# Performance work log

Hardware: AMD Instinct MI355X
Metric: run time of the kernel (lower is better)

## Reference

```python
import jax, jax.numpy as jnp
import numpy as np

MAX_LORAS, OUT, IN = 8, 4096, 4096
B, S = 4, 2048


def setup_inputs() -> dict:
    key = jax.random.key(0)
    k1, k2, k3 = jax.random.split(key, 3)
    x = jax.random.normal(k1, (B, S, IN), dtype=jnp.float32)
    weight = jax.random.normal(k2, (MAX_LORAS, OUT, IN), dtype=jnp.float32) * 0.02
    adapter_ids = jax.random.randint(k3, (B,), 0, MAX_LORAS, dtype=jnp.int32)
    return {"x": x, "weight": weight, "adapter_ids": adapter_ids}


def reference(x, weight, adapter_ids):
    # Gather a full [OUT, IN] matrix per batch element (matches weight[adapter_ids]).
    w = weight[adapter_ids]                 # [B, OUT, IN]
    # F.linear(x, w) == x @ w^T, batched over B: [B, S, IN] x [B, OUT, IN] -> [B, S, OUT]
    return jnp.einsum('bsi,boi->bso', x, w)
```

## Files before the change

### kernel.cpp

```cpp
#include <hip/hip_runtime.h>
#include <hip/hip_bf16.h>


#define SEQ    2048
#define IN_K   4096
#define OUT_N  4096
#define NB     4

typedef __attribute__((ext_vector_type(8))) short  short8;
typedef __attribute__((ext_vector_type(4))) float  float4v;

constexpr int BM = 256, BN = 256, BK = 32;
constexpr int GT = 512;
constexpr int KTILES = IN_K / BK;

__device__ inline short f2b(float f) {
    union { float f; unsigned u; } v; v.f = f;
    unsigned r = v.u + 0x7FFFu + ((v.u >> 16) & 1u);
    return (short)(r >> 16);
}
__device__ inline short8 pack8(float4v lo, float4v hi) {
    short8 r;
    r[0] = f2b(lo[0]); r[1] = f2b(lo[1]); r[2] = f2b(lo[2]); r[3] = f2b(lo[3]);
    r[4] = f2b(hi[0]); r[5] = f2b(hi[1]); r[6] = f2b(hi[2]); r[7] = f2b(hi[3]);
    return r;
}

typedef const __attribute__((address_space(1))) void* gp1_t;
typedef __attribute__((address_space(3))) void*       lp3_t;
__device__ inline void gload_lds16(const void* g, void* l) {
    __builtin_amdgcn_global_load_lds((gp1_t)g, (lp3_t)l, 16, 0, 0);
}

#define WAITV(N)  asm volatile("s_waitcnt vmcnt(" #N ")" ::: "memory")
#define WAITL0()  asm volatile("s_waitcnt lgkmcnt(0)" ::: "memory")

__global__ __launch_bounds__(256)
void cvt_x_kernel(const float* __restrict__ x, short* __restrict__ o, int n8)
{
    int i = blockIdx.x * blockDim.x + threadIdx.x;
    const int stride = gridDim.x * blockDim.x;
    for (; i < n8; i += stride) {
        const float4v a = *(const float4v*)(x + (size_t)i * 8);
        const float4v b = *(const float4v*)(x + (size_t)i * 8 + 4);
        *(short8*)(o + (size_t)i * 8) = pack8(a, b);
    }
}

__global__ __launch_bounds__(256)
void cvt_w_kernel(const float* __restrict__ w, const int* __restrict__ ids,
                  short* __restrict__ o, int by_id)
{
    const int b  = blockIdx.y;
    const int id = ids[b];
    int slot = b;
    if (by_id) {
        for (int j = 0; j < b; ++j) if (ids[j] == id) return;
        slot = id;
    }
    const float* __restrict__ src = w + (size_t)id   * OUT_N * IN_K;
    short* __restrict__       dst = o + (size_t)slot * OUT_N * IN_K;
    const int n8 = OUT_N * IN_K / 8;
    int i = blockIdx.x * blockDim.x + threadIdx.x;
    const int stride = gridDim.x * blockDim.x;
    for (; i < n8; i += stride) {
        const float4v a = *(const float4v*)(src + (size_t)i * 8);
        const float4v c = *(const float4v*)(src + (size_t)i * 8 + 4);
        *(short8*)(dst + (size_t)i * 8) = pack8(a, c);
    }
}

__global__ __launch_bounds__(GT, 2)
void mll_gemm_v5(const short* __restrict__ A, const short* __restrict__ W,
                 const int* __restrict__ ids, int by_id, float* __restrict__ out)
{
    __shared__ __align__(16) short lds[4][2 * BM * BK];

    const int tid  = threadIdx.x;
    const int lane = tid & 63;
    const int wid  = tid >> 6;
    const int wr   = wid >> 2;
    const int wc   = wid & 3;

    const int bid = blockIdx.x;
    const int n   = (bid & 7) * 64 + (bid >> 3);
    const int bx  = n & 15;
    const int by  = (n >> 4) & 7;
    const int bz  = n >> 7;
    const int brow = by * BM, bcol = bx * BN;

    const int wslot = by_id ? ids[bz] : bz;
    const short* __restrict__ Ab = A + (size_t)bz * SEQ * IN_K + (size_t)brow * IN_K;
    const short* __restrict__ Bb = W + (size_t)wslot * OUT_N * IN_K + (size_t)bcol * IN_K;

    const int c0 = tid, c1 = tid + GT;
    const int r0_ = c0 >> 2, s0_ = (c0 & 3) ^ ((r0_ >> 1) & 3);
    const int r1_ = c1 >> 2, s1_ = (c1 & 3) ^ ((r1_ >> 1) & 3);
    const short* pa0 = Ab + (size_t)r0_ * IN_K + s0_ * 8;
    const short* pa1 = Ab + (size_t)r1_ * IN_K + s1_ * 8;
    const short* pb0 = Bb + (size_t)r0_ * IN_K + s0_ * 8;
    const short* pb1 = Bb + (size_t)r1_ * IN_K + s1_ * 8;

    float4v acc[8][4];
#pragma unroll
    for (int m = 0; m < 8; ++m)
#pragma unroll
        for (int q = 0; q < 4; ++q)
            acc[m][q] = (float4v){0.f, 0.f, 0.f, 0.f};

    const int lr  = lane & 15;
    const int ksl = lane >> 4;
    const int ks2 = (ksl ^ ((lr >> 1) & 3)) * 8;

#pragma unroll
    for (int tt = 0; tt < 3; ++tt) {
        short* s = &lds[tt][0];
        gload_lds16(pa0 + tt * BK, s + c0 * 8);
        gload_lds16(pa1 + tt * BK, s + c1 * 8);
        gload_lds16(pb0 + tt * BK, s + BM * BK + c0 * 8);
        gload_lds16(pb1 + tt * BK, s + BM * BK + c1 * 8);
    }
    WAITV(8);
    __builtin_amdgcn_s_barrier();

    short8 af_a[4], af_b[4], bf[4];
    {
        const short* sA = &lds[0][0];
        const short* sB = sA + BM * BK;
#pragma unroll
        for (int m = 0; m < 4; ++m)
            af_a[m] = *(const short8*)(sA + (wr * 128 + m * 16 + lr) * BK + ks2);
#pragma unroll
        for (int q = 0; q < 4; ++q)
            bf[q] = *(const short8*)(sB + (wc * 64 + q * 16 + lr) * BK + ks2);
    }

    for (int t = 0; t < KTILES; ++t) {
        const short* sA = &lds[t & 3][0];

        WAITL0();
        __builtin_amdgcn_s_setprio(1);
#pragma unroll
        for (int m = 0; m < 4; ++m)
#pragma unroll
            for (int q = 0; q < 4; ++q)
                acc[m][q] = __builtin_amdgcn_mfma_f32_16x16x32_bf16(
                    af_a[m], bf[q], acc[m][q], 0, 0, 0);
        __builtin_amdgcn_s_setprio(0);
#pragma unroll
        for (int m = 0; m < 4; ++m)
            af_b[m] = *(const short8*)(sA + (wr * 128 + (m + 4) * 16 + lr) * BK + ks2);
        if (t <= KTILES - 4) {
            short* d = &lds[(t + 3) & 3][0];
            gload_lds16(pa0 + (t + 3) * BK, d + c0 * 8);
            gload_lds16(pa1 + (t + 3) * BK, d + c1 * 8);
        }
        if (t <= KTILES - 4)      WAITV(6);
        else if (t == KTILES - 3) WAITV(4);
        else if (t == KTILES - 2) WAITV(0);
        __builtin_amdgcn_s_barrier();

        WAITL0();
        __builtin_amdgcn_s_setprio(1);
#pragma unroll
        for (int m = 0; m < 4; ++m)
#pragma unroll
            for (int q = 0; q < 4; ++q)
                acc[m + 4][q] = __builtin_amdgcn_mfma_f32_16x16x32_bf16(
                    af_b[m], bf[q], acc[m + 4][q], 0, 0, 0);
        __builtin_amdgcn_s_setprio(0);
        if (t < KTILES - 1) {
            const short* sN = &lds[(t + 1) & 3][0];
            const short* sNB = sN + BM * BK;
#pragma unroll
            for (int m = 0; m < 4; ++m)
                af_a[m] = *(const short8*)(sN + (wr * 128 + m * 16 + lr) * BK + ks2);
#pragma unroll
            for (int q = 0; q < 4; ++q)
                bf[q] = *(const short8*)(sNB + (wc * 64 + q * 16 + lr) * BK + ks2);
        }
        if (t <= KTILES - 4) {
            short* d = &lds[(t + 3) & 3][0];
            gload_lds16(pb0 + (t + 3) * BK, d + BM * BK + c0 * 8);
            gload_lds16(pb1 + (t + 3) * BK, d + BM * BK + c1 * 8);
        }
        __builtin_amdgcn_s_barrier();
    }

    float* __restrict__ ob = out + (size_t)bz * SEQ * OUT_N;
    const int lrow = ksl * 4;
#pragma unroll
    for (int m = 0; m < 8; ++m) {
#pragma unroll
        for (int q = 0; q < 4; ++q) {
            const int r0 = brow + wr * 128 + m * 16 + lrow;
            const int c  = bcol + wc * 64 + q * 16 + lr;
#pragma unroll
            for (int j = 0; j < 4; ++j)
                ob[(size_t)(r0 + j) * OUT_N + c] = acc[m][q][j];
        }
    }
}

__device__ inline int xr(int row) { return (row & 3) ^ ((row >> 2) & 3); }

__global__ __launch_bounds__(256, 2)
void mll_gemm_fused(const float* __restrict__ x,
                    const float* __restrict__ w,
                    const int*   __restrict__ adapter_ids,
                    float* __restrict__ out)
{
    constexpr int FBM = 128, FBN = 128, FBK = 32;
    __shared__ __align__(16) short As[2][FBM * FBK];
    __shared__ __align__(16) short Bs[2][FBN * FBK];

    const int tid  = threadIdx.x;
    const int lane = tid & 63;
    const int wave = tid >> 6;
    const int wr   = wave >> 1;
    const int wc   = wave & 1;

    const int b    = blockIdx.z;
    const int aid  = adapter_ids[b];
    const int brow = blockIdx.y * FBM;
    const int bcol = blockIdx.x * FBN;

    const float* __restrict__ xb = x + (size_t)b   * SEQ   * IN_K;
    const float* __restrict__ wb = w + (size_t)aid * OUT_N * IN_K;

    float4v ra[2][2], rb[2][2];

    auto LOADG = [&](int kt) {
        const int k0 = kt * FBK;
#pragma unroll
        for (int g = 0; g < 2; ++g) {
            const int f  = tid + g * 256;
            const int r  = f >> 2;
            const int sl = f & 3;
            const float* pa = xb + (size_t)(brow + r) * IN_K + k0 + sl * 8;
            ra[g][0] = *(const float4v*)pa;
            ra[g][1] = *(const float4v*)(pa + 4);
            const float* pb = wb + (size_t)(bcol + r) * IN_K + k0 + sl * 8;
            rb[g][0] = *(const float4v*)pb;
            rb[g][1] = *(const float4v*)(pb + 4);
        }
    };
    auto STORE_LDS = [&](int buf) {
#pragma unroll
        for (int g = 0; g < 2; ++g) {
            const int f  = tid + g * 256;
            const int r  = f >> 2;
            const int sl = f & 3;
            const int ss = sl ^ xr(r);
            *(short8*)&As[buf][r * FBK + ss * 8] = pack8(ra[g][0], ra[g][1]);
            *(short8*)&Bs[buf][r * FBK + ss * 8] = pack8(rb[g][0], rb[g][1]);
        }
    };

    float4v acc[4][4];
#pragma unroll
    for (int m = 0; m < 4; ++m)
#pragma unroll
        for (int q = 0; q < 4; ++q)
            acc[m][q] = (float4v){0.f, 0.f, 0.f, 0.f};

    const int NT = IN_K / FBK;
    LOADG(0); STORE_LDS(0); __syncthreads();
    int cur = 0;
    for (int kt = 0; kt < NT; ++kt) {
        if (kt + 1 < NT) LOADG(kt + 1);
        short8 af[4], bfr[4];
        const int ksl = lane >> 4;
#pragma unroll
        for (int m = 0; m < 4; ++m) {
            const int rr = wr * 64 + m * 16 + (lane & 15);
            af[m] = *(const short8*)&As[cur][rr * FBK + (ksl ^ xr(rr)) * 8];
        }
#pragma unroll
        for (int q = 0; q < 4; ++q) {
            const int rc = wc * 64 + q * 16 + (lane & 15);
            bfr[q] = *(const short8*)&Bs[cur][rc * FBK + (ksl ^ xr(rc)) * 8];
        }
#pragma unroll
        for (int m = 0; m < 4; ++m)
#pragma unroll
            for (int q = 0; q < 4; ++q)
                acc[m][q] = __builtin_amdgcn_mfma_f32_16x16x32_bf16(
                    af[m], bfr[q], acc[m][q], 0, 0, 0);
        if (kt + 1 < NT) STORE_LDS(cur ^ 1);
        __syncthreads();
        cur ^= 1;
    }

    float* __restrict__ ob = out + (size_t)b * SEQ * OUT_N;
    const int lrow = (lane >> 4) * 4;
    const int lcol = lane & 15;
#pragma unroll
    for (int m = 0; m < 4; ++m) {
#pragma unroll
        for (int q = 0; q < 4; ++q) {
            const int r0 = brow + wr * 64 + m * 16 + lrow;
            const int c  = bcol + wc * 64 + q * 16 + lcol;
#pragma unroll
            for (int j = 0; j < 4; ++j)
                ob[(size_t)(r0 + j) * OUT_N + c] = acc[m][q][j];
        }
    }
}

extern "C" void kernel_launch(void* const* d_in, const int* in_sizes, int n_in,
                              void* d_out, int out_size, void* d_ws, size_t ws_size,
                              hipStream_t stream)
{
    const float* x   = (const float*)d_in[0];
    const float* w   = (const float*)d_in[1];
    const int*   ids = (const int*)d_in[2];
    float* out = (float*)d_out;

    const size_t xb_bytes   = (size_t)NB * SEQ   * IN_K * sizeof(short);
    const size_t wb4_bytes  = (size_t)NB * OUT_N * IN_K * sizeof(short);
    const size_t wb8_bytes  = (size_t)8  * OUT_N * IN_K * sizeof(short);

    if (ws_size >= xb_bytes + wb8_bytes) {
        short* xb16 = (short*)d_ws;
        short* wb16 = (short*)((char*)d_ws + xb_bytes);
        cvt_x_kernel<<<2048, 256, 0, stream>>>(x, xb16, NB * SEQ * IN_K / 8);
        cvt_w_kernel<<<dim3(1024, NB), 256, 0, stream>>>(w, ids, wb16, 1);
        mll_gemm_v5<<<512, GT, 0, stream>>>(xb16, wb16, ids, 1, out);
    } else if (ws_size >= xb_bytes + wb4_bytes) {
        short* xb16 = (short*)d_ws;
        short* wb16 = (short*)((char*)d_ws + xb_bytes);
        cvt_x_kernel<<<2048, 256, 0, stream>>>(x, xb16, NB * SEQ * IN_K / 8);
        cvt_w_kernel<<<dim3(1024, NB), 256, 0, stream>>>(w, ids, wb16, 0);
        mll_gemm_v5<<<512, GT, 0, stream>>>(xb16, wb16, ids, 0, out);
    } else {
        mll_gemm_fused<<<dim3(OUT_N / 128, SEQ / 128, NB), 256, 0, stream>>>(
            x, w, ids, out);
    }
}
```

Measured before the change: 336.8 us.

## Restructure GEMM main loop to single barrier per tile and remap blocks to XCDs

The K-loop now issues all four async global-to-LDS loads for tile t+3 up front, then runs all 32 MFMAs for the tile, and uses one barrier before loading all A/B fragments for the next tile. This replaces the two-half interleaved schedule with two barriers and explicit lgkmcnt waits. The block-to-tile mapping is also changed so each XCD pair handles one batch and contiguous column groups, aiming at better L2 locality of the shared weight and activation tiles. The cost is more live fragment registers (8 A fragments) and less overlap of LDS reads with MFMA, since fragment loads now follow the barrier.

```diff
diff --git a/kernel.cpp b/kernel.cpp
--- a/kernel.cpp
+++ b/kernel.cpp
@@ -33,7 +33,6 @@
 }
 
 #define WAITV(N)  asm volatile("s_waitcnt vmcnt(" #N ")" ::: "memory")
-#define WAITL0()  asm volatile("s_waitcnt lgkmcnt(0)" ::: "memory")
 
 __global__ __launch_bounds__(256)
 void cvt_x_kernel(const float* __restrict__ x, short* __restrict__ o, int n8)
@@ -71,7 +70,7 @@
 }
 
 __global__ __launch_bounds__(GT, 2)
-void mll_gemm_v5(const short* __restrict__ A, const short* __restrict__ W,
+void mll_gemm_v6(const short* __restrict__ A, const short* __restrict__ W,
                  const int* __restrict__ ids, int by_id, float* __restrict__ out)
 {
     __shared__ __align__(16) short lds[4][2 * BM * BK];
@@ -83,10 +82,13 @@
     const int wc   = wid & 3;
 
     const int bid = blockIdx.x;
-    const int n   = (bid & 7) * 64 + (bid >> 3);
-    const int bx  = n & 15;
-    const int by  = (n >> 4) & 7;
-    const int bz  = n >> 7;
+    const int xcd = bid & 7;
+    const int i_  = bid >> 3;
+    const int rr_ = i_ >> 5;
+    const int j_  = i_ & 31;
+    const int bz  = xcd >> 1;
+    const int bx  = (xcd & 1) * 8 + rr_ * 4 + (j_ >> 3);
+    const int by  = j_ & 7;
     const int brow = by * BM, bcol = bx * BN;
 
     const int wslot = by_id ? ids[bz] : bz;
@@ -112,6 +114,8 @@
     const int ksl = lane >> 4;
     const int ks2 = (ksl ^ ((lr >> 1) & 3)) * 8;
 
+    short8 af[8], bf[4];
+
 #pragma unroll
     for (int tt = 0; tt < 3; ++tt) {
         short* s = &lds[tt][0];
@@ -123,68 +127,50 @@
     WAITV(8);
     __builtin_amdgcn_s_barrier();
 
-    short8 af_a[4], af_b[4], bf[4];
     {
         const short* sA = &lds[0][0];
         const short* sB = sA + BM * BK;
 #pragma unroll
-        for (int m = 0; m < 4; ++m)
-            af_a[m] = *(const short8*)(sA + (wr * 128 + m * 16 + lr) * BK + ks2);
+        for (int m = 0; m < 8; ++m)
+            af[m] = *(const short8*)(sA + (wr * 128 + m * 16 + lr) * BK + ks2);
 #pragma unroll
         for (int q = 0; q < 4; ++q)
             bf[q] = *(const short8*)(sB + (wc * 64 + q * 16 + lr) * BK + ks2);
     }
 
     for (int t = 0; t < KTILES; ++t) {
-        const short* sA = &lds[t & 3][0];
-
-        WAITL0();
-        __builtin_amdgcn_s_setprio(1);
-#pragma unroll
-        for (int m = 0; m < 4; ++m)
-#pragma unroll
-            for (int q = 0; q < 4; ++q)
-                acc[m][q] = __builtin_amdgcn_mfma_f32_16x16x32_bf16(
-                    af_a[m], bf[q], acc[m][q], 0, 0, 0);
-        __builtin_amdgcn_s_setprio(0);
-#pragma unroll
-        for (int m = 0; m < 4; ++m)
-            af_b[m] = *(const short8*)(sA + (wr * 128 + (m + 4) * 16 + lr) * BK + ks2);
-        if (t <= KTILES - 4) {
+        if (t + 3 < KTILES) {
             short* d = &lds[(t + 3) & 3][0];
             gload_lds16(pa0 + (t + 3) * BK, d + c0 * 8);
             gload_lds16(pa1 + (t + 3) * BK, d + c1 * 8);
-        }
-        if (t <= KTILES - 4)      WAITV(6);
+            gload_lds16(pb0 + (t + 3) * BK, d + BM * BK + c0 * 8);
+            gload_lds16(pb1 + (t + 3) * BK, d + BM * BK + c1 * 8);
+        }
+
+        __builtin_amdgcn_s_setprio(1);
+#pragma unroll
+        for (int m = 0; m < 8; ++m)
+#pragma unroll
+            for (int q = 0; q < 4; ++q)
+                acc[m][q] = __builtin_amdgcn_mfma_f32_16x16x32_bf16(
+                    af[m], bf[q], acc[m][q], 0, 0, 0);
+        __builtin_amdgcn_s_setprio(0);
+
+        if (t <= KTILES - 4)      WAITV(8);
         else if (t == KTILES - 3) WAITV(4);
         else if (t == KTILES - 2) WAITV(0);
         __builtin_amdgcn_s_barrier();
 
-        WAITL0();
-        __builtin_amdgcn_s_setprio(1);
-#pragma unroll
-        for (int m = 0; m < 4; ++m)
+        if (t + 1 < KTILES) {
+            const short* sA = &lds[(t + 1) & 3][0];
+            const short* sB = sA + BM * BK;
+#pragma unroll
+            for (int m = 0; m < 8; ++m)
+                af[m] = *(const short8*)(sA + (wr * 128 + m * 16 + lr) * BK + ks2);
 #pragma unroll
             for (int q = 0; q < 4; ++q)
-                acc[m + 4][q] = __builtin_amdgcn_mfma_f32_16x16x32_bf16(
-                    af_b[m], bf[q], acc[m + 4][q], 0, 0, 0);
-        __builtin_amdgcn_s_setprio(0);
-        if (t < KTILES - 1) {
-            const short* sN = &lds[(t + 1) & 3][0];
-            const short* sNB = sN + BM * BK;
-#pragma unroll
-            for (int m = 0; m < 4; ++m)
-                af_a[m] = *(const short8*)(sN + (wr * 128 + m * 16 + lr) * BK + ks2);
-#pragma unroll
-            for (int q = 0; q < 4; ++q)
-                bf[q] = *(const short8*)(sNB + (wc * 64 + q * 16 + lr) * BK + ks2);
-        }
-        if (t <= KTILES - 4) {
-            short* d = &lds[(t + 3) & 3][0];
-            gload_lds16(pb0 + (t + 3) * BK, d + BM * BK + c0 * 8);
-            gload_lds16(pb1 + (t + 3) * BK, d + BM * BK + c1 * 8);
-        }
-        __builtin_amdgcn_s_barrier();
+                bf[q] = *(const short8*)(sB + (wc * 64 + q * 16 + lr) * BK + ks2);
+        }
     }
 
     float* __restrict__ ob = out + (size_t)bz * SEQ * OUT_N;
@@ -273,8 +259,8 @@
         const int ksl = lane >> 4;
 #pragma unroll
         for (int m = 0; m < 4; ++m) {
-            const int rr = wr * 64 + m * 16 + (lane & 15);
-            af[m] = *(const short8*)&As[cur][rr * FBK + (ksl ^ xr(rr)) * 8];
+            const int rrk = wr * 64 + m * 16 + (lane & 15);
+            af[m] = *(const short8*)&As[cur][rrk * FBK + (ksl ^ xr(rrk)) * 8];
         }
 #pragma unroll
         for (int q = 0; q < 4; ++q) {
@@ -326,13 +312,13 @@
         short* wb16 = (short*)((char*)d_ws + xb_bytes);
         cvt_x_kernel<<<2048, 256, 0, stream>>>(x, xb16, NB * SEQ * IN_K / 8);
         cvt_w_kernel<<<dim3(1024, NB), 256, 0, stream>>>(w, ids, wb16, 1);
-        mll_gemm_v5<<<512, GT, 0, stream>>>(xb16, wb16, ids, 1, out);
+        mll_gemm_v6<<<512, GT, 0, stream>>>(xb16, wb16, ids, 1, out);
     } else if (ws_size >= xb_bytes + wb4_bytes) {
         short* xb16 = (short*)d_ws;
         short* wb16 = (short*)((char*)d_ws + xb_bytes);
         cvt_x_kernel<<<2048, 256, 0, stream>>>(x, xb16, NB * SEQ * IN_K / 8);
         cvt_w_kernel<<<dim3(1024, NB), 256, 0, stream>>>(w, ids, wb16, 0);
-        mll_gemm_v5<<<512, GT, 0, stream>>>(xb16, wb16, ids, 0, out);
+        mll_gemm_v6<<<512, GT, 0, stream>>>(xb16, wb16, ids, 0, out);
     } else {
         mll_gemm_fused<<<dim3(OUT_N / 128, SEQ / 128, NB), 256, 0, stream>>>(
             x, w, ids, out);
```

New measurement: 348.0 us. +3.3%, slower.

## Fuse x fp32-to-bf16 conversion into GEMM A-tile loads

Applied to the files above, without the earlier changes.

Drops the separate x conversion kernel. The GEMM now reads fp32 x directly into registers two tiles ahead, packs it to bf16 and writes it to LDS, while W still streams through global_load_lds. This avoids writing and re-reading a bf16 copy of x (64MB read, 32MB write, 32MB re-read). The cost is that each block re-reads fp32 x across the 16 column tiles (twice the bytes of bf16), plus extra registers, VALU conversion work and changed vmcnt accounting in the pipeline.

```diff
diff --git a/kernel.cpp b/kernel.cpp
--- a/kernel.cpp
+++ b/kernel.cpp
@@ -34,18 +34,6 @@
 
 #define WAITV(N)  asm volatile("s_waitcnt vmcnt(" #N ")" ::: "memory")
 #define WAITL0()  asm volatile("s_waitcnt lgkmcnt(0)" ::: "memory")
-
-__global__ __launch_bounds__(256)
-void cvt_x_kernel(const float* __restrict__ x, short* __restrict__ o, int n8)
-{
-    int i = blockIdx.x * blockDim.x + threadIdx.x;
-    const int stride = gridDim.x * blockDim.x;
-    for (; i < n8; i += stride) {
-        const float4v a = *(const float4v*)(x + (size_t)i * 8);
-        const float4v b = *(const float4v*)(x + (size_t)i * 8 + 4);
-        *(short8*)(o + (size_t)i * 8) = pack8(a, b);
-    }
-}
 
 __global__ __launch_bounds__(256)
 void cvt_w_kernel(const float* __restrict__ w, const int* __restrict__ ids,
@@ -71,7 +59,7 @@
 }
 
 __global__ __launch_bounds__(GT, 2)
-void mll_gemm_v5(const short* __restrict__ A, const short* __restrict__ W,
+void mll_gemm_v8(const float* __restrict__ X, const short* __restrict__ W,
                  const int* __restrict__ ids, int by_id, float* __restrict__ out)
 {
     __shared__ __align__(16) short lds[4][2 * BM * BK];
@@ -90,14 +78,14 @@
     const int brow = by * BM, bcol = bx * BN;
 
     const int wslot = by_id ? ids[bz] : bz;
-    const short* __restrict__ Ab = A + (size_t)bz * SEQ * IN_K + (size_t)brow * IN_K;
+    const float* __restrict__ Xb = X + (size_t)bz * SEQ * IN_K + (size_t)brow * IN_K;
     const short* __restrict__ Bb = W + (size_t)wslot * OUT_N * IN_K + (size_t)bcol * IN_K;
 
     const int c0 = tid, c1 = tid + GT;
     const int r0_ = c0 >> 2, s0_ = (c0 & 3) ^ ((r0_ >> 1) & 3);
     const int r1_ = c1 >> 2, s1_ = (c1 & 3) ^ ((r1_ >> 1) & 3);
-    const short* pa0 = Ab + (size_t)r0_ * IN_K + s0_ * 8;
-    const short* pa1 = Ab + (size_t)r1_ * IN_K + s1_ * 8;
+    const float* qa0 = Xb + (size_t)r0_ * IN_K + s0_ * 8;
+    const float* qa1 = Xb + (size_t)r1_ * IN_K + s1_ * 8;
     const short* pb0 = Bb + (size_t)r0_ * IN_K + s0_ * 8;
     const short* pb1 = Bb + (size_t)r1_ * IN_K + s1_ * 8;
 
@@ -112,15 +100,53 @@
     const int ksl = lane >> 4;
     const int ks2 = (ksl ^ ((lr >> 1) & 3)) * 8;
 
-#pragma unroll
-    for (int tt = 0; tt < 3; ++tt) {
-        short* s = &lds[tt][0];
-        gload_lds16(pa0 + tt * BK, s + c0 * 8);
-        gload_lds16(pa1 + tt * BK, s + c1 * 8);
-        gload_lds16(pb0 + tt * BK, s + BM * BK + c0 * 8);
-        gload_lds16(pb1 + tt * BK, s + BM * BK + c1 * 8);
-    }
-    WAITV(8);
+    float4v rA[4];
+
+    auto LOADA = [&](int kt) {
+        const float* a0 = qa0 + kt * BK;
+        const float* a1 = qa1 + kt * BK;
+        rA[0] = *(const float4v*)a0;
+        rA[1] = *(const float4v*)(a0 + 4);
+        rA[2] = *(const float4v*)a1;
+        rA[3] = *(const float4v*)(a1 + 4);
+    };
+    auto WRITEA = [&](int kt) {
+        short* d = &lds[kt & 3][0];
+        *(short8*)(d + c0 * 8) = pack8(rA[0], rA[1]);
+        *(short8*)(d + c1 * 8) = pack8(rA[2], rA[3]);
+    };
+    auto GLOADB = [&](int kt) {
+        short* d = &lds[kt & 3][0] + BM * BK;
+        gload_lds16(pb0 + kt * BK, d + c0 * 8);
+        gload_lds16(pb1 + kt * BK, d + c1 * 8);
+    };
+
+    float4v rAa[4], rAb[4];
+    {
+        const float* a0 = qa0;
+        const float* a1 = qa1;
+        rAa[0] = *(const float4v*)a0;      rAa[1] = *(const float4v*)(a0 + 4);
+        rAa[2] = *(const float4v*)a1;      rAa[3] = *(const float4v*)(a1 + 4);
+        const float* b0 = qa0 + BK;
+        const float* b1 = qa1 + BK;
+        rAb[0] = *(const float4v*)b0;      rAb[1] = *(const float4v*)(b0 + 4);
+        rAb[2] = *(const float4v*)b1;      rAb[3] = *(const float4v*)(b1 + 4);
+    }
+    GLOADB(0); GLOADB(1); GLOADB(2);
+    WAITV(10);
+    {
+        short* d = &lds[0][0];
+        *(short8*)(d + c0 * 8) = pack8(rAa[0], rAa[1]);
+        *(short8*)(d + c1 * 8) = pack8(rAa[2], rAa[3]);
+    }
+    WAITV(6);
+    {
+        short* d = &lds[1][0];
+        *(short8*)(d + c0 * 8) = pack8(rAb[0], rAb[1]);
+        *(short8*)(d + c1 * 8) = pack8(rAb[2], rAb[3]);
+    }
+    WAITV(4);
+    WAITL0();
     __builtin_amdgcn_s_barrier();
 
     short8 af_a[4], af_b[4], bf[4];
@@ -150,17 +176,14 @@
 #pragma unroll
         for (int m = 0; m < 4; ++m)
             af_b[m] = *(const short8*)(sA + (wr * 128 + (m + 4) * 16 + lr) * BK + ks2);
-        if (t <= KTILES - 4) {
-            short* d = &lds[(t + 3) & 3][0];
-            gload_lds16(pa0 + (t + 3) * BK, d + c0 * 8);
-            gload_lds16(pa1 + (t + 3) * BK, d + c1 * 8);
-        }
-        if (t <= KTILES - 4)      WAITV(6);
-        else if (t == KTILES - 3) WAITV(4);
+
+        if (t <= KTILES - 3)      WAITV(2);
         else if (t == KTILES - 2) WAITV(0);
+        if (t >= 1 && t <= KTILES - 2) WRITEA(t + 1);
+        if (t + 2 < KTILES) LOADA(t + 2);
+        WAITL0();
         __builtin_amdgcn_s_barrier();
 
-        WAITL0();
         __builtin_amdgcn_s_setprio(1);
 #pragma unroll
         for (int m = 0; m < 4; ++m)
@@ -170,7 +193,7 @@
                     af_b[m], bf[q], acc[m + 4][q], 0, 0, 0);
         __builtin_amdgcn_s_setprio(0);
         if (t < KTILES - 1) {
-            const short* sN = &lds[(t + 1) & 3][0];
+            const short* sN  = &lds[(t + 1) & 3][0];
             const short* sNB = sN + BM * BK;
 #pragma unroll
             for (int m = 0; m < 4; ++m)
@@ -179,11 +202,7 @@
             for (int q = 0; q < 4; ++q)
                 bf[q] = *(const short8*)(sNB + (wc * 64 + q * 16 + lr) * BK + ks2);
         }
-        if (t <= KTILES - 4) {
-            short* d = &lds[(t + 3) & 3][0];
-            gload_lds16(pb0 + (t + 3) * BK, d + BM * BK + c0 * 8);
-            gload_lds16(pb1 + (t + 3) * BK, d + BM * BK + c1 * 8);
-        }
+        if (t + 3 < KTILES) GLOADB(t + 3);
         __builtin_amdgcn_s_barrier();
     }
 
@@ -273,8 +292,8 @@
         const int ksl = lane >> 4;
 #pragma unroll
         for (int m = 0; m < 4; ++m) {
-            const int rr = wr * 64 + m * 16 + (lane & 15);
-            af[m] = *(const short8*)&As[cur][rr * FBK + (ksl ^ xr(rr)) * 8];
+            const int rrk = wr * 64 + m * 16 + (lane & 15);
+            af[m] = *(const short8*)&As[cur][rrk * FBK + (ksl ^ xr(rrk)) * 8];
         }
 #pragma unroll
         for (int q = 0; q < 4; ++q) {
@@ -317,22 +336,17 @@
     const int*   ids = (const int*)d_in[2];
     float* out = (float*)d_out;
 
-    const size_t xb_bytes   = (size_t)NB * SEQ   * IN_K * sizeof(short);
-    const size_t wb4_bytes  = (size_t)NB * OUT_N * IN_K * sizeof(short);
-    const size_t wb8_bytes  = (size_t)8  * OUT_N * IN_K * sizeof(short);
-
-    if (ws_size >= xb_bytes + wb8_bytes) {
-        short* xb16 = (short*)d_ws;
-        short* wb16 = (short*)((char*)d_ws + xb_bytes);
-        cvt_x_kernel<<<2048, 256, 0, stream>>>(x, xb16, NB * SEQ * IN_K / 8);
+    const size_t wb4_bytes = (size_t)NB * OUT_N * IN_K * sizeof(short);
+    const size_t wb8_bytes = (size_t)8  * OUT_N * IN_K * sizeof(short);
+
+    if (ws_size >= wb8_bytes) {
+        short* wb16 = (short*)d_ws;
         cvt_w_kernel<<<dim3(1024, NB), 256, 0, stream>>>(w, ids, wb16, 1);
-        mll_gemm_v5<<<512, GT, 0, stream>>>(xb16, wb16, ids, 1, out);
-    } else if (ws_size >= xb_bytes + wb4_bytes) {
-        short* xb16 = (short*)d_ws;
-        short* wb16 = (short*)((char*)d_ws + xb_bytes);
-        cvt_x_kernel<<<2048, 256, 0, stream>>>(x, xb16, NB * SEQ * IN_K / 8);
+        mll_gemm_v8<<<512, GT, 0, stream>>>(x, wb16, ids, 1, out);
+    } else if (ws_size >= wb4_bytes) {
+        short* wb16 = (short*)d_ws;
         cvt_w_kernel<<<dim3(1024, NB), 256, 0, stream>>>(w, ids, wb16, 0);
-        mll_gemm_v5<<<512, GT, 0, stream>>>(xb16, wb16, ids, 0, out);
+        mll_gemm_v8<<<512, GT, 0, stream>>>(x, wb16, ids, 0, out);
     } else {
         mll_gemm_fused<<<dim3(OUT_N / 128, SEQ / 128, NB), 256, 0, stream>>>(
             x, w, ids, out);
```

Measured after the change: 376.3 us. 1.12x slower.
